# Optimization experiments

Measured on AMD Instinct MI355X. Metric: run time of the kernel, lower is better.

The kernel has to match this reference:

```python
import math
import jax, jax.numpy as jnp
import numpy as np

N, E, D, B, S, H = 16384, 196608, 256, 256, 64, 8
DH = D // H
BN_INV = 1.0 / math.sqrt(1.0 + 1e-5)  # eval-mode BN: mean=0, var=1, eps=1e-5
LOG2 = math.log(2.0)


def _mlp(x, w1, b1, w2, b2):
    # Linear -> SiLU -> Linear
    return jax.nn.silu(x @ w1 + b1) @ w2 + b2


def _bn(x, g, b):
    # BatchNorm1d in eval mode with running_mean=0, running_var=1
    return x * (BN_INV * g) + b


def _graph_ln(x, g, b):
    # pyg LayerNorm(mode='graph') called with batch=None: normalize over all nodes+features
    mu = jnp.mean(x)
    xc = x - mu
    var = jnp.mean(xc * xc)
    return xc * jax.lax.rsqrt(var + 1e-5) * g + b


def _forward(x, edge_index, edge_attr,
             node_w1, node_b1, node_w2, node_b2,
             c_w1, c_b1, c_w2, c_b2,
             bn_e_g, bn_e_b, bn_h_g, bn_h_b,
             n1l_g, n1l_b, n1a_g, n1a_b, n2_g, n2_b,
             wq, bq, wk, bk, wv, bv, wo, bo,
             aff_w1, aff_b1, aff_w2, aff_b2,
             fn_g, fn_b, fc_w1, fc_b1, fc_w2, fc_b2):
    row, col = edge_index[0], edge_index[1]

    # ---- PotNetConvGate local branch ----
    # A, B, V, U MLPs (all take node features) computed with stacked weights [4,D,D]
    hid = jax.nn.silu(jnp.einsum('nd,kdf->knf', x, node_w1) + node_b1[:, None, :])
    node_out = jnp.einsum('knf,kfg->kng', hid, node_w2) + node_b2[:, None, :]
    h_A, h_B, h_V, h_U = node_out[0], node_out[1], node_out[2], node_out[3]
    e_C = _mlp(edge_attr, c_w1, c_b1, c_w2, c_b2)  # [E,D]

    score = jax.nn.relu(_bn(h_A[row] + h_B[col] + e_C, bn_e_g, bn_e_b))  # [E,D]
    e_new = edge_attr + score

    # pyg softmax over edges grouped by destination node (col), per channel
    m = jax.ops.segment_max(e_new, col, num_segments=N)        # [N,D]
    ex = jnp.exp(e_new - m[col])
    s = jax.ops.segment_sum(ex, col, num_segments=N)           # [N,D]
    gated = ex / (s[col] + 1e-16)

    msg = gated * (h_V[col] + e_new)
    aggr = jax.ops.segment_sum(msg, col, num_segments=N)       # [N,D]
    h_local = jax.nn.silu(x + _bn(h_U + aggr, bn_h_g, bn_h_b))
    # e_out = silu(e_new + edge_attr)  # edge output, not used downstream for node output
    h_local = _bn(h_local, n1l_g, n1l_b)  # norm1_local

    # ---- global Transformer branch (equal-size graphs -> dense reshape, full mask) ----
    hd = x.reshape(B, S, D)
    q = (hd @ wq + bq).reshape(B, S, H, DH).transpose(0, 2, 1, 3)
    k = (hd @ wk + bk).reshape(B, S, H, DH).transpose(0, 2, 1, 3)
    v = (hd @ wv + bv).reshape(B, S, H, DH).transpose(0, 2, 1, 3)
    att = jax.nn.softmax(jnp.einsum('bhqd,bhkd->bhqk', q, k) / math.sqrt(DH), axis=-1)
    o = jnp.einsum('bhqk,bhkd->bhqd', att, v).transpose(0, 2, 1, 3).reshape(B, S, D)
    h_attn = (o @ wo + bo).reshape(N, D)

    h_attn = _bn(h_attn + x, n1a_g, n1a_b)  # norm1_attn
    t = jax.nn.gelu(h_attn @ aff_w1 + aff_b1, approximate=False) @ aff_w2 + aff_b2
    h_attn = _graph_ln(t + x, fn_g, fn_b)   # feed_norm

    # ---- fuse branches (mean over stacked outputs) ----
    h_new = (h_local + h_attn) * 0.5

    # ---- _ff_block: fc = Linear -> ShiftedSoftplus -> Linear ----
    ssp = jax.nn.softplus(h_new @ fc_w1 + fc_b1) - LOG2
    out = ssp @ fc_w2 + fc_b2
    return _bn(out + h_new, n2_g, n2_b)  # norm2


def setup_inputs():
    key = jax.random.key(0)
    ks = iter(jax.random.split(key, 64))
    sc = 1.0 / math.sqrt(D)
    def w(shape):
        return jax.random.normal(next(ks), shape, jnp.float32) * sc
    z = lambda *s: jnp.zeros(s, jnp.float32)
    o = lambda *s: jnp.ones(s, jnp.float32)
    return {
        'x': jax.random.normal(next(ks), (N, D), jnp.float32),
        'edge_index': jax.random.randint(next(ks), (2, E), 0, N, jnp.int32),
        'edge_attr': jax.random.normal(next(ks), (E, D), jnp.float32),
        'node_w1': w((4, D, D)), 'node_b1': z(4, D),
        'node_w2': w((4, D, D)), 'node_b2': z(4, D),
        'c_w1': w((D, D)), 'c_b1': z(D), 'c_w2': w((D, D)), 'c_b2': z(D),
        'bn_e_g': o(D), 'bn_e_b': z(D), 'bn_h_g': o(D), 'bn_h_b': z(D),
        'n1l_g': o(D), 'n1l_b': z(D), 'n1a_g': o(D), 'n1a_b': z(D),
        'n2_g': o(D), 'n2_b': z(D),
        'wq': w((D, D)), 'bq': z(D), 'wk': w((D, D)), 'bk': z(D),
        'wv': w((D, D)), 'bv': z(D), 'wo': w((D, D)), 'bo': z(D),
        'aff_w1': w((D, 2 * D)), 'aff_b1': z(2 * D),
        'aff_w2': w((2 * D, D)), 'aff_b2': z(D),
        'fn_g': o(D), 'fn_b': z(D),
        'fc_w1': w((D, 2 * D)), 'fc_b1': z(2 * D),
        'fc_w2': w((2 * D, D)), 'fc_b2': z(D),
    }


def reference(x, edge_index, edge_attr,
              node_w1, node_b1, node_w2, node_b2,
              c_w1, c_b1, c_w2, c_b2,
              bn_e_g, bn_e_b, bn_h_g, bn_h_b,
              n1l_g, n1l_b, n1a_g, n1a_b, n2_g, n2_b,
              wq, bq, wk, bk, wv, bv, wo, bo,
              aff_w1, aff_b1, aff_w2, aff_b2,
              fn_g, fn_b, fc_w1, fc_b1, fc_w2, fc_b2):
    return _forward(x, edge_index, edge_attr,
                    node_w1, node_b1, node_w2, node_b2,
                    c_w1, c_b1, c_w2, c_b2,
                    bn_e_g, bn_e_b, bn_h_g, bn_h_b,
                    n1l_g, n1l_b, n1a_g, n1a_b, n2_g, n2_b,
                    wq, bq, wk, bk, wv, bv, wo, bo,
                    aff_w1, aff_b1, aff_w2, aff_b2,
                    fn_g, fn_b, fc_w1, fc_b1, fc_w2, fc_b2)
```

## Files before the change

### kernel.cpp

```cpp
#include <hip/hip_runtime.h>
#include <hip/hip_bf16.h>
#include <stdint.h>

#define NN 16384
#define NE 196608
#define DD 256
#define ND 4194304
#define ECH 65536
#define BNINV 0.9999950000374997f
#define LOG2F_ 0.6931471805599453f

typedef __attribute__((ext_vector_type(8))) short short8v;
typedef __attribute__((ext_vector_type(4))) float float4v;

__device__ __forceinline__ float b2f(__hip_bfloat16 v) { return __bfloat162float(v); }
__device__ __forceinline__ __hip_bfloat16 f2b(float v) { return __float2bfloat16(v); }

__device__ __forceinline__ void gl_lds16(const __hip_bfloat16* g, __hip_bfloat16* l) {
  __builtin_amdgcn_global_load_lds((const __attribute__((address_space(1))) void*)g,
                                   (__attribute__((address_space(3))) void*)l, 16, 0, 0);
}

__device__ __forceinline__ float rdf(const void* p, size_t i, int fl) {
  return fl ? b2f(((const __hip_bfloat16*)p)[i]) : ((const float*)p)[i];
}

#define OFF_WT    0ul
#define OFF_PB    2883584ul
#define OFF_XB    2899968ul
#define OFF_HIDE  11288576ul
#define OFF_HNEWB 44843008ul
#define OFF_HN    53231616ul
#define OFF_HL    86786048ul
#define OFF_EN    120340480ul
#define OFF_QKV   120340480ul
#define OFF_O     170672128ul
#define OFF_HATTN 179060736ul
#define OFF_U     187449344ul
#define OFF_HNEW  204226560ul
#define OFF_TAIL  221003776ul

#define PB_NB1   0
#define PB_NB2   1024
#define PB_CB1   2048
#define PB_CB2   2304
#define PB_QKVB  2560
#define PB_BO    3328
#define PB_AB1   3584
#define PB_AB2   4096
#define PB_FB1   4352
#define PB_FB2   4864
#define PB_BNEG  5120
#define PB_BNEB  5376
#define PB_BNHG  5632
#define PB_BNHB  5888
#define PB_N1LG  6144
#define PB_N1LB  6400
#define PB_N1AG  6656
#define PB_N1AB  6912
#define PB_N2G   7168
#define PB_N2B   7424
#define PB_FNG   7680
#define PB_FNB   7936

__global__ void probe_kernel(const uint32_t* bneg_raw, int* flag) {
  if (threadIdx.x == 0 && blockIdx.x == 0)
    *flag = (bneg_raw[0] == 0x3F803F80u) ? 1 : 0;
}

struct PJobs {
  const void* src[24];
  int off[24];
  int len[24];
};

__global__ void canon_params(PJobs jb, __hip_bfloat16* PB, const int* flagp) {
  const int fl = *flagp;
  const int j = blockIdx.x;
  const void* src = jb.src[j];
  const int off = jb.off[j], len = jb.len[j];
  for (int i = threadIdx.x; i < len; i += 256) PB[off + i] = f2b(rdf(src, i, fl));
}

__global__ void canon_x(const void* x, __hip_bfloat16* XB, const int* flagp) {
  const int fl = *flagp;
  const size_t i = (size_t)blockIdx.x * 256 + threadIdx.x;
  XB[i] = f2b(rdf(x, i, fl));
}

struct TJobsF {
  const void* src[18];
  __hip_bfloat16* dst[18];
  int R[18];
  int C[18];
  int RB[18];
};

__global__ void transpose_rb(TJobsF jb, const int* flagp) {
  __shared__ __hip_bfloat16 tile[32][33];
  const int fl = *flagp;
  const int j = blockIdx.z;
  const int R = jb.R[j], C = jb.C[j], RB = jb.RB[j];
  const int c0 = blockIdx.x * 32, r0 = blockIdx.y * 32;
  if (c0 >= C || r0 >= R) return;
  const void* src = jb.src[j];
  __hip_bfloat16* dst = jb.dst[j];
  const int tx = threadIdx.x, ty = threadIdx.y;
#pragma unroll
  for (int i = 0; i < 4; ++i)
    tile[ty + i * 8][tx] = f2b(rdf(src, (size_t)(RB + r0 + ty + i * 8) * C + c0 + tx, fl));
  __syncthreads();
#pragma unroll
  for (int i = 0; i < 4; ++i)
    dst[(long)(c0 + ty + i * 8) * R + r0 + tx] = tile[tx][ty + i * 8];
}

__global__ void prep_kernel(int* counts, double* stats) {
  const int i = blockIdx.x * blockDim.x + threadIdx.x;
  if (i < NN) counts[i] = 0;
  if (i == 0) counts[NN] = 0;
  if (i < 2) stats[i] = 0.0;
}

template <int ACT, int RES, int BNM, int OUTBF, int ASRC, int DUALOUT>
__global__ __launch_bounds__(256) void gemm_bt(
    const void* __restrict__ Avp, const __hip_bfloat16* __restrict__ Wt,
    const __hip_bfloat16* __restrict__ bias, const void* __restrict__ Res,
    const __hip_bfloat16* __restrict__ bng, const __hip_bfloat16* __restrict__ bnb,
    void* __restrict__ Cout, const int* __restrict__ flagp,
    int M, int N, int K, long boff, long az, long wz, long bz, long cz) {
  __shared__ __align__(16) __hip_bfloat16 sA[128 * 32];
  __shared__ __align__(16) __hip_bfloat16 sB[128 * 32];
  const int fl = (ASRC || DUALOUT) ? *flagp : 1;
  const int z = blockIdx.z;
  const long aoff = boff + (long)z * az;
  const __hip_bfloat16* Ab = (const __hip_bfloat16*)Avp + aoff;
  const float* Af = (const float*)Avp + aoff;
  Wt += (long)z * wz;
  bias += (long)z * bz;
  const long coff = (long)z * cz;
  const int tid = threadIdx.x;
  const int lane = tid & 63;
  const int wid = tid >> 6;
  const int wm = wid >> 1, wn = wid & 1;
  const int l16 = lane & 15, lq = lane >> 4;
  const long am0 = (long)blockIdx.y * 128;
  const long bn0 = (long)blockIdx.x * 128;

  float4v acc[4][4] = {};

  const int nK = K >> 5;
  for (int kb = 0; kb < nK; ++kb) {
    if (ASRC == 1 && fl == 0) {
#pragma unroll
      for (int r = 0; r < 2; ++r) {
        const int c = tid + r * 256;
        const float* ap = Af + (am0 + (c >> 2)) * K + kb * 32 + (c & 3) * 8;
        const float4v f0 = *(const float4v*)ap;
        const float4v f1 = *(const float4v*)(ap + 4);
        short8v s;
#pragma unroll
        for (int i = 0; i < 4; ++i) {
          __hip_bfloat16 h0 = f2b(f0[i]), h1 = f2b(f1[i]);
          s[i] = *(short*)&h0;
          s[4 + i] = *(short*)&h1;
        }
        ((short8v*)sA)[c] = s;
        gl_lds16(Wt + (bn0 + (c >> 2)) * K + kb * 32 + (c & 3) * 8, sB + c * 8);
      }
    } else {
#pragma unroll
      for (int r = 0; r < 2; ++r) {
        const int c = tid + r * 256;
        gl_lds16(Ab + (am0 + (c >> 2)) * K + kb * 32 + (c & 3) * 8, sA + c * 8);
        gl_lds16(Wt + (bn0 + (c >> 2)) * K + kb * 32 + (c & 3) * 8, sB + c * 8);
      }
    }
    __syncthreads();
    const short* pA = (const short*)sA;
    const short* pB = (const short*)sB;
    short8v af[4], bv_[4];
#pragma unroll
    for (int mi = 0; mi < 4; ++mi)
      af[mi] = *(const short8v*)(pA + (wm * 64 + mi * 16 + l16) * 32 + lq * 8);
#pragma unroll
    for (int ni = 0; ni < 4; ++ni)
      bv_[ni] = *(const short8v*)(pB + (wn * 64 + ni * 16 + l16) * 32 + lq * 8);
#pragma unroll
    for (int mi = 0; mi < 4; ++mi)
#pragma unroll
      for (int ni = 0; ni < 4; ++ni)
        acc[mi][ni] =
            __builtin_amdgcn_mfma_f32_16x16x32_bf16(af[mi], bv_[ni], acc[mi][ni], 0, 0, 0);
    __syncthreads();
  }

  const __hip_bfloat16* Rb = (const __hip_bfloat16*)Res;
  const float* Rf = (const float*)Res;
#pragma unroll
  for (int mi = 0; mi < 4; ++mi) {
#pragma unroll
    for (int ni = 0; ni < 4; ++ni) {
#pragma unroll
      for (int r = 0; r < 4; ++r) {
        const long row = am0 + wm * 64 + mi * 16 + lq * 4 + r;
        const long col = bn0 + wn * 64 + ni * 16 + l16;
        float v = acc[mi][ni][r] + b2f(bias[col]);
        if (ACT == 1) v = v / (1.f + expf(-v));
        else if (ACT == 2) v = 0.5f * v * (1.f + erff(v * 0.7071067811865476f));
        else if (ACT == 3) v = (v > 15.f ? v : log1pf(expf(v))) - LOG2F_;
        if (RES == 1) v += b2f(Rb[row * N + col]);
        else if (RES == 2) v += Rf[row * N + col];
        if (BNM) v = v * (BNINV * b2f(bng[col])) + b2f(bnb[col]);
        if (DUALOUT) {
          if (fl) ((__hip_bfloat16*)Cout)[coff + row * N + col] = f2b(v);
          else ((float*)Cout)[coff + row * N + col] = v;
        } else if (OUTBF) {
          ((__hip_bfloat16*)Cout)[coff + row * N + col] = f2b(v);
        } else {
          ((float*)Cout)[coff + row * N + col] = v;
        }
      }
    }
  }
}

__global__ __launch_bounds__(256) void gemm_edge2(
    const __hip_bfloat16* __restrict__ A, const __hip_bfloat16* __restrict__ Wt,
    const __hip_bfloat16* __restrict__ bias, const int* __restrict__ ei,
    const void* __restrict__ eattr, const __hip_bfloat16* __restrict__ HA,
    __hip_bfloat16* __restrict__ EN, const __hip_bfloat16* __restrict__ PB,
    const int* __restrict__ flagp, long ebase) {
  __shared__ __align__(16) __hip_bfloat16 sA[128 * 32];
  __shared__ __align__(16) __hip_bfloat16 sB[128 * 32];
  const int fl = *flagp;
  const int tid = threadIdx.x;
  const int lane = tid & 63;
  const int wid = tid >> 6;
  const int wm = wid >> 1, wn = wid & 1;
  const int l16 = lane & 15, lq = lane >> 4;
  const long am0 = (long)blockIdx.y * 128;
  const long bn0 = (long)blockIdx.x * 128;
  const __hip_bfloat16* HB = HA + (size_t)ND;

  float4v acc[4][4] = {};

  const int K = DD;
  for (int kb = 0; kb < (K >> 5); ++kb) {
#pragma unroll
    for (int r = 0; r < 2; ++r) {
      const int c = tid + r * 256;
      gl_lds16(A + (am0 + (c >> 2)) * K + kb * 32 + (c & 3) * 8, sA + c * 8);
      gl_lds16(Wt + (bn0 + (c >> 2)) * K + kb * 32 + (c & 3) * 8, sB + c * 8);
    }
    __syncthreads();
    const short* pA = (const short*)sA;
    const short* pB = (const short*)sB;
    short8v af[4], bv_[4];
#pragma unroll
    for (int mi = 0; mi < 4; ++mi)
      af[mi] = *(const short8v*)(pA + (wm * 64 + mi * 16 + l16) * 32 + lq * 8);
#pragma unroll
    for (int ni = 0; ni < 4; ++ni)
      bv_[ni] = *(const short8v*)(pB + (wn * 64 + ni * 16 + l16) * 32 + lq * 8);
#pragma unroll
    for (int mi = 0; mi < 4; ++mi)
#pragma unroll
      for (int ni = 0; ni < 4; ++ni)
        acc[mi][ni] =
            __builtin_amdgcn_mfma_f32_16x16x32_bf16(af[mi], bv_[ni], acc[mi][ni], 0, 0, 0);
    __syncthreads();
  }

#pragma unroll
  for (int mi = 0; mi < 4; ++mi) {
#pragma unroll
    for (int r = 0; r < 4; ++r) {
      const long row = am0 + wm * 64 + mi * 16 + lq * 4 + r;
      const long ge = ebase + row;
      const int rr = ei[ge];
      const int cc = ei[NE + ge];
#pragma unroll
      for (int ni = 0; ni < 4; ++ni) {
        const long col = bn0 + wn * 64 + ni * 16 + l16;
        float v = acc[mi][ni][r] + b2f(bias[col]);
        v += b2f(HA[(size_t)rr * DD + col]) + b2f(HB[(size_t)cc * DD + col]);
        v = v * (BNINV * b2f(PB[PB_BNEG + col])) + b2f(PB[PB_BNEB + col]);
        v = fmaxf(v, 0.f);
        v += rdf(eattr, (size_t)ge * DD + col, fl);
        EN[(size_t)ge * DD + col] = f2b(v);
      }
    }
  }
}

__global__ void count_kernel(const int* __restrict__ ei, int* __restrict__ counts) {
  const int e = blockIdx.x * 256 + threadIdx.x;
  if (e < NE) atomicAdd(&counts[ei[NE + e]], 1);
}

__global__ __launch_bounds__(1024) void scan_kernel(int* __restrict__ counts,
                                                    int* __restrict__ cursor) {
  __shared__ int part[1024];
  const int t = threadIdx.x;
  const int base = t * 16;
  int ss = 0;
#pragma unroll
  for (int i = 0; i < 16; ++i) ss += counts[base + i];
  part[t] = ss;
  __syncthreads();
  for (int off = 1; off < 1024; off <<= 1) {
    int v = (t >= off) ? part[t - off] : 0;
    __syncthreads();
    part[t] += v;
    __syncthreads();
  }
  int run = part[t] - ss;
  for (int i = 0; i < 16; ++i) {
    const int cv = counts[base + i];
    counts[base + i] = run;
    cursor[base + i] = run;
    run += cv;
  }
  if (t == 1023) counts[NN] = run;
}

__global__ void scatter_kernel(const int* __restrict__ ei, int* __restrict__ cursor,
                               int* __restrict__ eids) {
  const int e = blockIdx.x * 256 + threadIdx.x;
  if (e < NE) {
    const int p = atomicAdd(&cursor[ei[NE + e]], 1);
    eids[p] = e;
  }
}

__global__ __launch_bounds__(256) void segment_kernel(
    const int* __restrict__ offs, const int* __restrict__ eids,
    const __hip_bfloat16* __restrict__ EN, const __hip_bfloat16* __restrict__ hV,
    const __hip_bfloat16* __restrict__ hU, const __hip_bfloat16* __restrict__ XB,
    const __hip_bfloat16* __restrict__ PB, float* __restrict__ hlocal) {
  __shared__ int sEid[256];
  const int n = blockIdx.x;
  const int d = threadIdx.x;
  const int beg = offs[n], end = offs[n + 1];
  float sa = 0.f, sb = 0.f;
  for (int base = beg; base < end; base += 256) {
    const int cnt = min(256, end - base);
    __syncthreads();
    if (threadIdx.x < cnt) sEid[threadIdx.x] = eids[base + threadIdx.x];
    __syncthreads();
    for (int i = 0; i < cnt; ++i) {
      const float v = b2f(EN[(size_t)sEid[i] * DD + d]);
      const float e = expf(v);
      sa += e;
      sb += e * v;
    }
  }
  const float hv = b2f(hV[(size_t)n * DD + d]);
  const float ag = (hv * sa + sb) / (sa + 1e-16f);
  const float t1 =
      (b2f(hU[(size_t)n * DD + d]) + ag) * (BNINV * b2f(PB[PB_BNHG + d])) + b2f(PB[PB_BNHB + d]);
  float s1 = b2f(XB[(size_t)n * DD + d]) + t1;
  s1 = s1 / (1.f + expf(-s1));
  s1 = s1 * (BNINV * b2f(PB[PB_N1LG + d])) + b2f(PB[PB_N1LB + d]);
  hlocal[(size_t)n * DD + d] = s1;
}

__global__ __launch_bounds__(256) void attn_kernel(const float* __restrict__ QKV,
                                                   __hip_bfloat16* __restrict__ O) {
  __shared__ float sq[64][33], sk[64][33], sv[64][33];
  __shared__ float sp[64][65];
  const int bh = blockIdx.x;
  const int b = bh >> 3, h = bh & 7;
  const int tid = threadIdx.x;
  const float* Q = QKV;
  const float* Kp = QKV + (size_t)ND;
  const float* Vp = QKV + 2 * (size_t)ND;
#pragma unroll
  for (int j = 0; j < 8; ++j) {
    const int idx = j * 256 + tid;
    const int s = idx >> 5, dh = idx & 31;
    const size_t ga = ((size_t)(b * 64 + s)) * DD + h * 32 + dh;
    sq[s][dh] = Q[ga];
    sk[s][dh] = Kp[ga];
    sv[s][dh] = Vp[ga];
  }
  __syncthreads();
  const int row = tid >> 2, l4 = tid & 3;
  float qr[32];
#pragma unroll
  for (int d = 0; d < 32; ++d) qr[d] = sq[row][d];
  float sc[16];
  float mx = -1e30f;
#pragma unroll
  for (int jj = 0; jj < 16; ++jj) {
    const int j = l4 * 16 + jj;
    float dot = 0.f;
#pragma unroll
    for (int d = 0; d < 32; ++d) dot += qr[d] * sk[j][d];
    dot *= 0.17677669529663687f;
    sc[jj] = dot;
    mx = fmaxf(mx, dot);
  }
  mx = fmaxf(mx, __shfl_xor(mx, 1));
  mx = fmaxf(mx, __shfl_xor(mx, 2));
  float se = 0.f;
#pragma unroll
  for (int jj = 0; jj < 16; ++jj) {
    sc[jj] = expf(sc[jj] - mx);
    se += sc[jj];
  }
  se += __shfl_xor(se, 1);
  se += __shfl_xor(se, 2);
  const float inv = 1.f / se;
#pragma unroll
  for (int jj = 0; jj < 16; ++jj) sp[row][l4 * 16 + jj] = sc[jj] * inv;
  __syncthreads();
#pragma unroll
  for (int k8 = 0; k8 < 8; ++k8) {
    const int dh = l4 * 8 + k8;
    float acc = 0.f;
#pragma unroll
    for (int j = 0; j < 64; ++j) acc += sp[row][j] * sv[j][dh];
    O[((size_t)(b * 64 + row)) * DD + h * 32 + dh] = f2b(acc);
  }
}

__global__ __launch_bounds__(256) void stats_kernel(const float* __restrict__ U,
                                                    double* __restrict__ st) {
  double s = 0.0, s2 = 0.0;
  for (size_t i = (size_t)blockIdx.x * 256 + threadIdx.x; i < (size_t)ND;
       i += (size_t)gridDim.x * 256) {
    const double v = (double)U[i];
    s += v;
    s2 += v * v;
  }
  for (int o = 32; o > 0; o >>= 1) {
    s += __shfl_down(s, o);
    s2 += __shfl_down(s2, o);
  }
  __shared__ double wred[4][2];
  const int lane = threadIdx.x & 63, w = threadIdx.x >> 6;
  if (lane == 0) {
    wred[w][0] = s;
    wred[w][1] = s2;
  }
  __syncthreads();
  if (threadIdx.x == 0) {
    double a = 0, bb = 0;
    for (int i = 0; i < 4; ++i) {
      a += wred[i][0];
      bb += wred[i][1];
    }
    atomicAdd(&st[0], a);
    atomicAdd(&st[1], bb);
  }
}

__global__ void finalize_stats(double* st) {
  if (threadIdx.x == 0 && blockIdx.x == 0) {
    const double mu = st[0] / (double)ND;
    const double var = st[1] / (double)ND - mu * mu;
    float* f = (float*)(st + 2);
    f[0] = (float)mu;
    f[1] = (float)(1.0 / sqrt(var + 1e-5));
  }
}

__global__ void hnew_kernel(const float* __restrict__ U, const float* __restrict__ hlocal,
                            const double* __restrict__ st, const __hip_bfloat16* __restrict__ PB,
                            float* __restrict__ HNEW, __hip_bfloat16* __restrict__ HNEWB) {
  const size_t i = (size_t)blockIdx.x * 256 + threadIdx.x;
  const float* f = (const float*)(st + 2);
  const float mu = f[0], rs = f[1];
  const int d = (int)(i & 255);
  const float ha = (U[i] - mu) * rs * b2f(PB[PB_FNG + d]) + b2f(PB[PB_FNB + d]);
  const float hn = 0.5f * (hlocal[i] + ha);
  HNEW[i] = hn;
  HNEWB[i] = f2b(hn);
}

extern "C" void kernel_launch(void* const* d_in, const int* in_sizes, int n_in, void* d_out,
                              int out_size, void* d_ws, size_t ws_size, hipStream_t stream) {
  (void)in_sizes; (void)n_in; (void)out_size; (void)ws_size;
  const void* x = d_in[0];
  const int* ei = (const int*)d_in[1];
  const void* eattr = d_in[2];

  uint8_t* ws = (uint8_t*)d_ws;
  __hip_bfloat16* WT = (__hip_bfloat16*)(ws + OFF_WT);
  __hip_bfloat16* PB = (__hip_bfloat16*)(ws + OFF_PB);
  __hip_bfloat16* XB = (__hip_bfloat16*)(ws + OFF_XB);
  __hip_bfloat16* HIDE = (__hip_bfloat16*)(ws + OFF_HIDE);
  __hip_bfloat16* HNEWB = (__hip_bfloat16*)(ws + OFF_HNEWB);
  __hip_bfloat16* HN = (__hip_bfloat16*)(ws + OFF_HN);
  float* HL = (float*)(ws + OFF_HL);
  __hip_bfloat16* EN = (__hip_bfloat16*)(ws + OFF_EN);
  float* QKV = (float*)(ws + OFF_QKV);
  __hip_bfloat16* O = (__hip_bfloat16*)(ws + OFF_O);
  __hip_bfloat16* HATTN = (__hip_bfloat16*)(ws + OFF_HATTN);
  float* U = (float*)(ws + OFF_U);
  float* HNEW = (float*)(ws + OFF_HNEW);
  uint8_t* tail = ws + OFF_TAIL;
  int* counts = (int*)tail;
  int* cursor = (int*)(tail + 66048ul);
  int* eids = (int*)(tail + 132096ul);
  double* stats = (double*)(tail + 918528ul);
  int* flag = (int*)(tail + 918592ul);

  probe_kernel<<<1, 64, 0, stream>>>((const uint32_t*)d_in[11], flag);

  PJobs pj;
  {
    const int srcidx[24] = {4, 6, 8, 10, 22, 24, 26, 28, 30, 32, 36, 38,
                            11, 12, 13, 14, 15, 16, 17, 18, 19, 20, 33, 34};
    const int dstoff[24] = {PB_NB1, PB_NB2, PB_CB1, PB_CB2, PB_QKVB, PB_QKVB + 256,
                            PB_QKVB + 512, PB_BO, PB_AB1, PB_AB2, PB_FB1, PB_FB2,
                            PB_BNEG, PB_BNEB, PB_BNHG, PB_BNHB, PB_N1LG, PB_N1LB,
                            PB_N1AG, PB_N1AB, PB_N2G, PB_N2B, PB_FNG, PB_FNB};
    const int lens[24] = {1024, 1024, 256, 256, 256, 256, 256, 256, 512, 256, 512, 256,
                          256, 256, 256, 256, 256, 256, 256, 256, 256, 256, 256, 256};
    for (int i = 0; i < 24; ++i) {
      pj.src[i] = d_in[srcidx[i]];
      pj.off[i] = dstoff[i];
      pj.len[i] = lens[i];
    }
  }
  canon_params<<<24, 256, 0, stream>>>(pj, PB, flag);
  canon_x<<<NN, 256, 0, stream>>>(x, XB, flag);

  TJobsF jf;
  for (int j = 0; j < 4; ++j) {
    jf.src[j] = d_in[3]; jf.dst[j] = WT + j * 65536;
    jf.R[j] = 256; jf.C[j] = 256; jf.RB[j] = j * 256;
    jf.src[4 + j] = d_in[5]; jf.dst[4 + j] = WT + 262144 + j * 65536;
    jf.R[4 + j] = 256; jf.C[4 + j] = 256; jf.RB[4 + j] = j * 256;
  }
  {
    const int widx[10] = {7, 9, 21, 23, 25, 27, 29, 31, 35, 37};
    const long wdst[10] = {524288, 589824, 655360, 720896, 786432, 851968,
                           917504, 1048576, 1179648, 1310720};
    const int wR[10] = {256, 256, 256, 256, 256, 256, 256, 512, 256, 512};
    const int wC[10] = {256, 256, 256, 256, 256, 256, 512, 256, 512, 256};
    for (int j = 0; j < 10; ++j) {
      jf.src[8 + j] = d_in[widx[j]]; jf.dst[8 + j] = WT + wdst[j];
      jf.R[8 + j] = wR[j]; jf.C[8 + j] = wC[j]; jf.RB[8 + j] = 0;
    }
  }
  transpose_rb<<<dim3(16, 16, 18), dim3(32, 8), 0, stream>>>(jf, flag);

  prep_kernel<<<64, 256, 0, stream>>>(counts, stats);

  count_kernel<<<768, 256, 0, stream>>>(ei, counts);
  scan_kernel<<<1, 1024, 0, stream>>>(counts, cursor);
  scatter_kernel<<<768, 256, 0, stream>>>(ei, cursor, eids);

  gemm_bt<1, 0, 0, 1, 0, 0><<<dim3(2, 128, 4), 256, 0, stream>>>(
      XB, WT, PB + PB_NB1, nullptr, nullptr, nullptr, HIDE, flag,
      NN, DD, DD, 0, 0, 65536, 256, ND);
  gemm_bt<0, 0, 0, 1, 0, 0><<<dim3(2, 128, 4), 256, 0, stream>>>(
      HIDE, WT + 262144, PB + PB_NB2, nullptr, nullptr, nullptr, HN, flag,
      NN, DD, DD, 0, ND, 65536, 256, ND);

  for (int ch = 0; ch < 3; ++ch) {
    const long eo = (long)ch * ECH * DD;
    gemm_bt<1, 0, 0, 1, 1, 0><<<dim3(2, 512, 1), 256, 0, stream>>>(
        eattr, WT + 524288, PB + PB_CB1, nullptr, nullptr, nullptr, HIDE, flag,
        ECH, DD, DD, eo, 0, 0, 0, 0);
    gemm_edge2<<<dim3(2, 512, 1), 256, 0, stream>>>(
        HIDE, WT + 589824, PB + PB_CB2, ei, eattr, HN, EN, PB, flag, (long)ch * ECH);
  }

  segment_kernel<<<NN, 256, 0, stream>>>(counts, eids, EN, HN + 2 * (size_t)ND,
                                         HN + 3 * (size_t)ND, XB, PB, HL);

  gemm_bt<0, 0, 0, 0, 0, 0><<<dim3(2, 128, 3), 256, 0, stream>>>(
      XB, WT + 655360, PB + PB_QKVB, nullptr, nullptr, nullptr, QKV, flag,
      NN, DD, DD, 0, 0, 65536, 256, ND);
  attn_kernel<<<2048, 256, 0, stream>>>(QKV, O);
  gemm_bt<0, 1, 1, 1, 0, 0><<<dim3(2, 128, 1), 256, 0, stream>>>(
      O, WT + 851968, PB + PB_BO, XB, PB + PB_N1AG, PB + PB_N1AB, HATTN, flag,
      NN, DD, DD, 0, 0, 0, 0, 0);

  gemm_bt<2, 0, 0, 1, 0, 0><<<dim3(4, 128, 1), 256, 0, stream>>>(
      HATTN, WT + 917504, PB + PB_AB1, nullptr, nullptr, nullptr, HIDE, flag,
      NN, 512, DD, 0, 0, 0, 0, 0);
  gemm_bt<0, 1, 0, 0, 0, 0><<<dim3(2, 128, 1), 256, 0, stream>>>(
      HIDE, WT + 1048576, PB + PB_AB2, XB, nullptr, nullptr, U, flag,
      NN, DD, 512, 0, 0, 0, 0, 0);

  stats_kernel<<<1024, 256, 0, stream>>>(U, stats);
  finalize_stats<<<1, 64, 0, stream>>>(stats);
  hnew_kernel<<<NN, 256, 0, stream>>>(U, HL, stats, PB, HNEW, HNEWB);

  gemm_bt<3, 0, 0, 1, 0, 0><<<dim3(4, 128, 1), 256, 0, stream>>>(
      HNEWB, WT + 1179648, PB + PB_FB1, nullptr, nullptr, nullptr, HIDE, flag,
      NN, 512, DD, 0, 0, 0, 0, 0);
  gemm_bt<0, 2, 1, 1, 0, 1><<<dim3(2, 128, 1), 256, 0, stream>>>(
      HIDE, WT + 1310720, PB + PB_FB2, HNEW, PB + PB_N2G, PB + PB_N2B, d_out, flag,
      NN, DD, 512, 0, 0, 0, 0, 0);
}
```

Baseline: 1.037 ms.

## Write edge features in destination-sorted order and merge edge GEMM chunks

The edge-score kernel now writes each edge row to its position in a destination-sorted permutation, so the segment softmax kernel reads contiguous rows instead of gathering through an edge-id list. The three chunked edge GEMM launches are merged into one full-size launch, using a larger workspace with separate hidden buffers. Accurate expf calls are also replaced with fast __expf, which slightly lowers accuracy. The scattered writes in the GEMM epilogue may cost some write coalescing.

```diff
diff --git a/kernel.cpp b/kernel.cpp
--- a/kernel.cpp
+++ b/kernel.cpp
@@ -6,7 +6,6 @@
 #define NE 196608
 #define DD 256
 #define ND 4194304
-#define ECH 65536
 #define BNINV 0.9999950000374997f
 #define LOG2F_ 0.6931471805599453f
 
@@ -28,17 +27,18 @@
 #define OFF_WT    0ul
 #define OFF_PB    2883584ul
 #define OFF_XB    2899968ul
-#define OFF_HIDE  11288576ul
-#define OFF_HNEWB 44843008ul
-#define OFF_HN    53231616ul
-#define OFF_HL    86786048ul
-#define OFF_EN    120340480ul
-#define OFF_QKV   120340480ul
-#define OFF_O     170672128ul
-#define OFF_HATTN 179060736ul
-#define OFF_U     187449344ul
-#define OFF_HNEW  204226560ul
-#define OFF_TAIL  221003776ul
+#define OFF_HN    11288576ul
+#define OFF_HL    44843008ul
+#define OFF_HIDE  61620224ul
+#define OFF_EN    162283520ul
+#define OFF_QKV   262946816ul
+#define OFF_O     313278464ul
+#define OFF_HATTN 321667072ul
+#define OFF_HIDN  330055680ul
+#define OFF_U     346832896ul
+#define OFF_HNEW  363610112ul
+#define OFF_HNEWB 380387328ul
+#define OFF_TAIL  388775936ul
 
 #define PB_NB1   0
 #define PB_NB2   1024
@@ -206,9 +206,9 @@
         const long row = am0 + wm * 64 + mi * 16 + lq * 4 + r;
         const long col = bn0 + wn * 64 + ni * 16 + l16;
         float v = acc[mi][ni][r] + b2f(bias[col]);
-        if (ACT == 1) v = v / (1.f + expf(-v));
+        if (ACT == 1) v = v / (1.f + __expf(-v));
         else if (ACT == 2) v = 0.5f * v * (1.f + erff(v * 0.7071067811865476f));
-        else if (ACT == 3) v = (v > 15.f ? v : log1pf(expf(v))) - LOG2F_;
+        else if (ACT == 3) v = (v > 15.f ? v : log1pf(__expf(v))) - LOG2F_;
         if (RES == 1) v += b2f(Rb[row * N + col]);
         else if (RES == 2) v += Rf[row * N + col];
         if (BNM) v = v * (BNINV * b2f(bng[col])) + b2f(bnb[col]);
@@ -230,7 +230,7 @@
     const __hip_bfloat16* __restrict__ bias, const int* __restrict__ ei,
     const void* __restrict__ eattr, const __hip_bfloat16* __restrict__ HA,
     __hip_bfloat16* __restrict__ EN, const __hip_bfloat16* __restrict__ PB,
-    const int* __restrict__ flagp, long ebase) {
+    const int* __restrict__ perm, const int* __restrict__ flagp) {
   __shared__ __align__(16) __hip_bfloat16 sA[128 * 32];
   __shared__ __align__(16) __hip_bfloat16 sB[128 * 32];
   const int fl = *flagp;
@@ -277,9 +277,10 @@
 #pragma unroll
     for (int r = 0; r < 4; ++r) {
       const long row = am0 + wm * 64 + mi * 16 + lq * 4 + r;
-      const long ge = ebase + row;
+      const long ge = row;
       const int rr = ei[ge];
       const int cc = ei[NE + ge];
+      const long pe = perm[ge];
 #pragma unroll
       for (int ni = 0; ni < 4; ++ni) {
         const long col = bn0 + wn * 64 + ni * 16 + l16;
@@ -288,7 +289,7 @@
         v = v * (BNINV * b2f(PB[PB_BNEG + col])) + b2f(PB[PB_BNEB + col]);
         v = fmaxf(v, 0.f);
         v += rdf(eattr, (size_t)ge * DD + col, fl);
-        EN[(size_t)ge * DD + col] = f2b(v);
+        EN[(size_t)pe * DD + col] = f2b(v);
       }
     }
   }
@@ -326,42 +327,45 @@
 }
 
 __global__ void scatter_kernel(const int* __restrict__ ei, int* __restrict__ cursor,
-                               int* __restrict__ eids) {
+                               int* __restrict__ perm) {
   const int e = blockIdx.x * 256 + threadIdx.x;
   if (e < NE) {
     const int p = atomicAdd(&cursor[ei[NE + e]], 1);
-    eids[p] = e;
+    perm[e] = p;
   }
 }
 
 __global__ __launch_bounds__(256) void segment_kernel(
-    const int* __restrict__ offs, const int* __restrict__ eids,
-    const __hip_bfloat16* __restrict__ EN, const __hip_bfloat16* __restrict__ hV,
-    const __hip_bfloat16* __restrict__ hU, const __hip_bfloat16* __restrict__ XB,
-    const __hip_bfloat16* __restrict__ PB, float* __restrict__ hlocal) {
-  __shared__ int sEid[256];
+    const int* __restrict__ offs, const __hip_bfloat16* __restrict__ EN,
+    const __hip_bfloat16* __restrict__ hV, const __hip_bfloat16* __restrict__ hU,
+    const __hip_bfloat16* __restrict__ XB, const __hip_bfloat16* __restrict__ PB,
+    float* __restrict__ hlocal) {
   const int n = blockIdx.x;
   const int d = threadIdx.x;
   const int beg = offs[n], end = offs[n + 1];
   float sa = 0.f, sb = 0.f;
-  for (int base = beg; base < end; base += 256) {
-    const int cnt = min(256, end - base);
-    __syncthreads();
-    if (threadIdx.x < cnt) sEid[threadIdx.x] = eids[base + threadIdx.x];
-    __syncthreads();
-    for (int i = 0; i < cnt; ++i) {
-      const float v = b2f(EN[(size_t)sEid[i] * DD + d]);
-      const float e = expf(v);
-      sa += e;
-      sb += e * v;
-    }
+  int p = beg;
+  for (; p + 4 <= end; p += 4) {
+    const float v0 = b2f(EN[(size_t)(p + 0) * DD + d]);
+    const float v1 = b2f(EN[(size_t)(p + 1) * DD + d]);
+    const float v2 = b2f(EN[(size_t)(p + 2) * DD + d]);
+    const float v3 = b2f(EN[(size_t)(p + 3) * DD + d]);
+    const float e0 = __expf(v0), e1 = __expf(v1), e2 = __expf(v2), e3 = __expf(v3);
+    sa += (e0 + e1) + (e2 + e3);
+    sb += (e0 * v0 + e1 * v1) + (e2 * v2 + e3 * v3);
+  }
+  for (; p < end; ++p) {
+    const float v = b2f(EN[(size_t)p * DD + d]);
+    const float e = __expf(v);
+    sa += e;
+    sb += e * v;
   }
   const float hv = b2f(hV[(size_t)n * DD + d]);
   const float ag = (hv * sa + sb) / (sa + 1e-16f);
   const float t1 =
       (b2f(hU[(size_t)n * DD + d]) + ag) * (BNINV * b2f(PB[PB_BNHG + d])) + b2f(PB[PB_BNHB + d]);
   float s1 = b2f(XB[(size_t)n * DD + d]) + t1;
-  s1 = s1 / (1.f + expf(-s1));
+  s1 = s1 / (1.f + __expf(-s1));
   s1 = s1 * (BNINV * b2f(PB[PB_N1LG + d])) + b2f(PB[PB_N1LB + d]);
   hlocal[(size_t)n * DD + d] = s1;
 }
@@ -407,7 +411,7 @@
   float se = 0.f;
 #pragma unroll
   for (int jj = 0; jj < 16; ++jj) {
-    sc[jj] = expf(sc[jj] - mx);
+    sc[jj] = __expf(sc[jj] - mx);
     se += sc[jj];
   }
   se += __shfl_xor(se, 1);
@@ -491,20 +495,21 @@
   __hip_bfloat16* WT = (__hip_bfloat16*)(ws + OFF_WT);
   __hip_bfloat16* PB = (__hip_bfloat16*)(ws + OFF_PB);
   __hip_bfloat16* XB = (__hip_bfloat16*)(ws + OFF_XB);
-  __hip_bfloat16* HIDE = (__hip_bfloat16*)(ws + OFF_HIDE);
-  __hip_bfloat16* HNEWB = (__hip_bfloat16*)(ws + OFF_HNEWB);
   __hip_bfloat16* HN = (__hip_bfloat16*)(ws + OFF_HN);
   float* HL = (float*)(ws + OFF_HL);
+  __hip_bfloat16* HIDE = (__hip_bfloat16*)(ws + OFF_HIDE);
   __hip_bfloat16* EN = (__hip_bfloat16*)(ws + OFF_EN);
   float* QKV = (float*)(ws + OFF_QKV);
   __hip_bfloat16* O = (__hip_bfloat16*)(ws + OFF_O);
   __hip_bfloat16* HATTN = (__hip_bfloat16*)(ws + OFF_HATTN);
+  __hip_bfloat16* HIDN = (__hip_bfloat16*)(ws + OFF_HIDN);
   float* U = (float*)(ws + OFF_U);
   float* HNEW = (float*)(ws + OFF_HNEW);
+  __hip_bfloat16* HNEWB = (__hip_bfloat16*)(ws + OFF_HNEWB);
   uint8_t* tail = ws + OFF_TAIL;
   int* counts = (int*)tail;
   int* cursor = (int*)(tail + 66048ul);
-  int* eids = (int*)(tail + 132096ul);
+  int* perm = (int*)(tail + 132096ul);
   double* stats = (double*)(tail + 918528ul);
   int* flag = (int*)(tail + 918592ul);
 
@@ -553,7 +558,7 @@
 
   count_kernel<<<768, 256, 0, stream>>>(ei, counts);
   scan_kernel<<<1, 1024, 0, stream>>>(counts, cursor);
-  scatter_kernel<<<768, 256, 0, stream>>>(ei, cursor, eids);
+  scatter_kernel<<<768, 256, 0, stream>>>(ei, cursor, perm);
 
   gemm_bt<1, 0, 0, 1, 0, 0><<<dim3(2, 128, 4), 256, 0, stream>>>(
       XB, WT, PB + PB_NB1, nullptr, nullptr, nullptr, HIDE, flag,
@@ -562,16 +567,13 @@
       HIDE, WT + 262144, PB + PB_NB2, nullptr, nullptr, nullptr, HN, flag,
       NN, DD, DD, 0, ND, 65536, 256, ND);
 
-  for (int ch = 0; ch < 3; ++ch) {
-    const long eo = (long)ch * ECH * DD;
-    gemm_bt<1, 0, 0, 1, 1, 0><<<dim3(2, 512, 1), 256, 0, stream>>>(
-        eattr, WT + 524288, PB + PB_CB1, nullptr, nullptr, nullptr, HIDE, flag,
-        ECH, DD, DD, eo, 0, 0, 0, 0);
-    gemm_edge2<<<dim3(2, 512, 1), 256, 0, stream>>>(
-        HIDE, WT + 589824, PB + PB_CB2, ei, eattr, HN, EN, PB, flag, (long)ch * ECH);
-  }
-
-  segment_kernel<<<NN, 256, 0, stream>>>(counts, eids, EN, HN + 2 * (size_t)ND,
+  gemm_bt<1, 0, 0, 1, 1, 0><<<dim3(2, 1536, 1), 256, 0, stream>>>(
+      eattr, WT + 524288, PB + PB_CB1, nullptr, nullptr, nullptr, HIDE, flag,
+      NE, DD, DD, 0, 0, 0, 0, 0);
+  gemm_edge2<<<dim3(2, 1536, 1), 256, 0, stream>>>(
+      HIDE, WT + 589824, PB + PB_CB2, ei, eattr, HN, EN, PB, perm, flag);
+
+  segment_kernel<<<NN, 256, 0, stream>>>(counts, EN, HN + 2 * (size_t)ND,
                                          HN + 3 * (size_t)ND, XB, PB, HL);
 
   gemm_bt<0, 0, 0, 0, 0, 0><<<dim3(2, 128, 3), 256, 0, stream>>>(
@@ -583,10 +585,10 @@
       NN, DD, DD, 0, 0, 0, 0, 0);
 
   gemm_bt<2, 0, 0, 1, 0, 0><<<dim3(4, 128, 1), 256, 0, stream>>>(
-      HATTN, WT + 917504, PB + PB_AB1, nullptr, nullptr, nullptr, HIDE, flag,
+      HATTN, WT + 917504, PB + PB_AB1, nullptr, nullptr, nullptr, HIDN, flag,
       NN, 512, DD, 0, 0, 0, 0, 0);
   gemm_bt<0, 1, 0, 0, 0, 0><<<dim3(2, 128, 1), 256, 0, stream>>>(
-      HIDE, WT + 1048576, PB + PB_AB2, XB, nullptr, nullptr, U, flag,
+      HIDN, WT + 1048576, PB + PB_AB2, XB, nullptr, nullptr, U, flag,
       NN, DD, 512, 0, 0, 0, 0, 0);
 
   stats_kernel<<<1024, 256, 0, stream>>>(U, stats);
@@ -594,9 +596,9 @@
   hnew_kernel<<<NN, 256, 0, stream>>>(U, HL, stats, PB, HNEW, HNEWB);
 
   gemm_bt<3, 0, 0, 1, 0, 0><<<dim3(4, 128, 1), 256, 0, stream>>>(
-      HNEWB, WT + 1179648, PB + PB_FB1, nullptr, nullptr, nullptr, HIDE, flag,
+      HNEWB, WT + 1179648, PB + PB_FB1, nullptr, nullptr, nullptr, HIDN, flag,
       NN, 512, DD, 0, 0, 0, 0, 0);
   gemm_bt<0, 2, 1, 1, 0, 1><<<dim3(2, 128, 1), 256, 0, stream>>>(
-      HIDE, WT + 1310720, PB + PB_FB2, HNEW, PB + PB_N2G, PB + PB_N2B, d_out, flag,
+      HIDN, WT + 1310720, PB + PB_FB2, HNEW, PB + PB_N2G, PB + PB_N2B, d_out, flag,
       NN, DD, 512, 0, 0, 0, 0, 0);
 }
```

Result: faster. 994.4 us (-4.1%).
